# Kernel optimization log

Hardware: AMD Instinct MI355X
Metric: run time of the kernel (lower is better)

The kernel has to match this reference:

```python
import jax, jax.numpy as jnp
import numpy as np

N_NODES, N_EDGES = 16384, 8192
IN_CH, HID_CH = 256, 256
ALPHA, BETA = -1.5, -0.5


def setup_inputs() -> dict:
    key = jax.random.key(0)
    k1, k2, k3, k4, k5, k6 = jax.random.split(key, 6)
    x_0 = jax.random.normal(k1, (N_NODES, IN_CH), dtype=jnp.float32)
    # binary incidence matrix (n_nodes, n_edges)
    incidence_1 = jax.random.randint(k2, (N_NODES, N_EDGES), 0, 2).astype(jnp.float32)
    # conv weights (torch Conv: x @ W then neighborhood @ .)
    W0 = jax.random.normal(k3, (IN_CH, HID_CH), dtype=jnp.float32) * 0.02
    W1 = jax.random.normal(k4, (HID_CH, HID_CH), dtype=jnp.float32) * 0.02
    # xavier_uniform biases of shape (1, hidden)
    gain = 1.414
    bound = gain * np.sqrt(6.0 / (1 + HID_CH)) * np.sqrt(3.0) / np.sqrt(3.0)  # xavier bound = gain*sqrt(6/(fan_in+fan_out))
    bound = gain * np.sqrt(6.0 / (1 + HID_CH))
    bias_0_to_1 = jax.random.uniform(k5, (1, HID_CH), minval=-bound, maxval=bound, dtype=jnp.float32)
    bias_1_to_0 = jax.random.uniform(k6, (1, HID_CH), minval=-bound, maxval=bound, dtype=jnp.float32)
    return {"x_0": x_0, "incidence_1": incidence_1, "W0": W0, "W1": W1,
            "bias_0_to_1": bias_0_to_1, "bias_1_to_0": bias_1_to_0}


def _normalize_incidence(B1):
    # edge/node cardinalities raised to alpha/beta
    edge_card = jnp.sum(B1, axis=0) ** ALPHA          # (n_edges,)
    node_card = jnp.sum(B1, axis=1) ** BETA           # (n_nodes,)
    mask = (B1 > 0).astype(B1.dtype)
    d0_inv = 1.0 / (mask @ edge_card)                 # (n_nodes,) per-node sum of incident edge_card
    d1_inv = 1.0 / (mask.T @ node_card)               # (n_edges,) per-edge sum of member node_card
    # B1_norm = D0_left^-1 @ B1 @ diag(edge_card)
    B1_norm = d0_inv[:, None] * B1 * edge_card[None, :]
    # B1T_norm = D1_left^-1 @ B1^T @ diag(node_card)
    B1T_norm = d1_inv[:, None] * B1.T * node_card[None, :]
    return B1_norm, B1T_norm


def reference(x_0, incidence_1, W0, W1, bias_0_to_1, bias_1_to_0):
    B1_norm, B1T_norm = _normalize_incidence(incidence_1)
    # node -> edge conv: x_1 = B1T_norm @ (x_0 @ W0) + b01
    x_1 = B1T_norm @ (x_0 @ W0) + bias_0_to_1        # (n_edges, hid)
    # edge -> node conv: x_0 = B1_norm @ (x_1 @ W1) + b10
    x_0_out = B1_norm @ (x_1 @ W1) + bias_1_to_0     # (n_nodes, hid)
    return jax.nn.relu(x_0_out), jax.nn.relu(x_1)
```

## Files before the change

kernel.cpp:

```cpp
#include <hip/hip_runtime.h>
#include <stdint.h>

#define NN 16384
#define NE 8192
#define CH 256
#define MM1_SPLIT 8
#define MM2_SPLIT 4

typedef __attribute__((ext_vector_type(8))) short bf16x8;
typedef __attribute__((ext_vector_type(4))) float f32x4;

__device__ __forceinline__ unsigned short f2bf(float f) {
  unsigned u = __float_as_uint(f);
  u += 0x7FFFu + ((u >> 16) & 1u);
  return (unsigned short)(u >> 16);
}
__device__ __forceinline__ void async_copy16(const void* gptr, void* lptr) {
  __builtin_amdgcn_global_load_lds((const __attribute__((address_space(1))) unsigned int*)gptr,
                                   (__attribute__((address_space(3))) unsigned int*)lptr,
                                   16, 0, 0);
}

__device__ __forceinline__ void transpose32(unsigned* x) {
  const unsigned masks[5] = {0x0000FFFFu, 0x00FF00FFu, 0x0F0F0F0Fu, 0x33333333u, 0x55555555u};
#pragma unroll
  for (int jj = 0; jj < 5; ++jj) {
    const int j = 16 >> jj;
    const unsigned m = masks[jj];
#pragma unroll
    for (int k = 0; k < 32; ++k) {
      if ((k & j) == 0) {
        unsigned t = ((x[k] >> j) ^ x[k + j]) & m;
        x[k] ^= (t << j);
        x[k + j] ^= t;
      }
    }
  }
}

__global__ void k0_transpose_w(const float* __restrict__ W0, const float* __restrict__ W1,
                               unsigned short* __restrict__ W0T, unsigned short* __restrict__ W1T) {
  const float* W = blockIdx.y ? W1 : W0;
  unsigned short* WT = blockIdx.y ? W1T : W0T;
  int n = blockIdx.x;
  int k = threadIdx.x;
  WT[n * CH + k] = f2bf(W[k * CH + n]);
}

__global__ void k1_pack_card(const float* __restrict__ B1, unsigned* __restrict__ pk1,
                             float* __restrict__ node_card) {
  int n = blockIdx.x;
  int t = threadIdx.x;
  const float4* p = (const float4*)(B1 + (size_t)n * NE + t * 32);
  unsigned w = 0;
#pragma unroll
  for (int jj = 0; jj < 8; ++jj) {
    float4 v = p[jj];
    w |= ((__float_as_uint(v.x) >> 23) & 1u) << (4 * jj);
    w |= ((__float_as_uint(v.y) >> 23) & 1u) << (4 * jj + 1);
    w |= ((__float_as_uint(v.z) >> 23) & 1u) << (4 * jj + 2);
    w |= ((__float_as_uint(v.w) >> 23) & 1u) << (4 * jj + 3);
  }
  pk1[(size_t)n * 256 + t] = w;
  int s = __popc(w);
  __shared__ int red[4];
#pragma unroll
  for (int off = 32; off; off >>= 1) s += __shfl_down(s, off, 64);
  if ((t & 63) == 0) red[t >> 6] = s;
  __syncthreads();
  if (t == 0) {
    float tot = (float)(red[0] + red[1] + red[2] + red[3]);
    node_card[n] = rsqrtf(tot);
  }
}

__global__ __launch_bounds__(256) void k1b_bitT(const unsigned* __restrict__ pk1,
                                                unsigned* __restrict__ pk1T) {
  int bw = blockIdx.x & 127;
  int half = blockIdx.x >> 7;
  int t = threadIdx.x;
  int nt = half * 256 + t;
  unsigned x0[32], x1[32];
#pragma unroll
  for (int r = 0; r < 32; ++r) {
    uint2 v = *(const uint2*)&pk1[(size_t)(nt * 32 + r) * 256 + 2 * bw];
    x0[r] = v.x;
    x1[r] = v.y;
  }
  transpose32(x0);
  transpose32(x1);
  int e0 = bw * 64;
#pragma unroll
  for (int c = 0; c < 32; ++c) {
    pk1T[(size_t)(e0 + c) * 512 + nt] = x0[c];
    pk1T[(size_t)(e0 + 32 + c) * 512 + nt] = x1[c];
  }
}

__global__ void kcs_edge_card(const unsigned* __restrict__ pk1T, float* __restrict__ edge_card) {
  int lane = threadIdx.x & 63;
  int e = blockIdx.x * 4 + (threadIdx.x >> 6);
  const uint4* p = (const uint4*)(pk1T + (size_t)e * 512) + lane * 2;
  uint4 a = p[0], b = p[1];
  int s = __popc(a.x) + __popc(a.y) + __popc(a.z) + __popc(a.w) +
          __popc(b.x) + __popc(b.y) + __popc(b.z) + __popc(b.w);
#pragma unroll
  for (int off = 32; off; off >>= 1) s += __shfl_down(s, off, 64);
  if (lane == 0) {
    float cs = (float)s;
    edge_card[e] = 1.0f / (cs * sqrtf(cs));
  }
}

__global__ __launch_bounds__(256) void k2_y0(const float* __restrict__ X0,
                                             const unsigned short* __restrict__ W0T,
                                             const float* __restrict__ node_card,
                                             unsigned short* __restrict__ y0sT) {
  __shared__ __align__(16) unsigned short a_lds[64 * 32];
  __shared__ __align__(16) unsigned short b_lds[256 * 32];
  const int tid = threadIdx.x;
  const int wave = tid >> 6, lane = tid & 63;
  const int quad = lane >> 4, l15 = lane & 15;
  const int m0 = blockIdx.x * 64;
  const int ar = tid >> 3, ac = (tid & 7) * 4;

  f32x4 acc[4][4];
  const f32x4 fz = {0.f, 0.f, 0.f, 0.f};
#pragma unroll
  for (int i = 0; i < 4; ++i)
#pragma unroll
    for (int j = 0; j < 4; ++j) acc[i][j] = fz;

  for (int k0 = 0; k0 < CH; k0 += 32) {
    __syncthreads();
#pragma unroll
    for (int p = 0; p < 2; ++p) {
      float4 v = *(const float4*)(X0 + (size_t)(m0 + ar + p * 32) * CH + k0 + ac);
      uint2 w;
      w.x = ((unsigned)f2bf(v.x)) | ((unsigned)f2bf(v.y) << 16);
      w.y = ((unsigned)f2bf(v.z)) | ((unsigned)f2bf(v.w) << 16);
      *(uint2*)&a_lds[(ar + p * 32) * 32 + ac] = w;
    }
#pragma unroll
    for (int i = 0; i < 4; ++i) {
      int rowbase = wave * 64 + i * 16;
      const unsigned short* g = W0T + (size_t)(rowbase + (lane >> 2)) * CH + k0 + (lane & 3) * 8;
      async_copy16(g, &b_lds[rowbase * 32]);
    }
    __syncthreads();
    bf16x8 af[4];
#pragma unroll
    for (int i = 0; i < 4; ++i)
      af[i] = *(const bf16x8*)&a_lds[(i * 16 + l15) * 32 + quad * 8];
#pragma unroll
    for (int j = 0; j < 4; ++j) {
      bf16x8 bfr = *(const bf16x8*)&b_lds[(wave * 64 + j * 16 + l15) * 32 + quad * 8];
#pragma unroll
      for (int i = 0; i < 4; ++i)
        acc[i][j] = __builtin_amdgcn_mfma_f32_16x16x32_bf16(af[i], bfr, acc[i][j], 0, 0, 0);
    }
  }
#pragma unroll
  for (int i = 0; i < 4; ++i) {
    int row4 = m0 + i * 16 + quad * 4;
    float4 nc = *(const float4*)(node_card + row4);
#pragma unroll
    for (int j = 0; j < 4; ++j) {
      int col = wave * 64 + j * 16 + l15;
      f32x4 v = acc[i][j];
      ushort4 o;
      o.x = f2bf(v[0] * nc.x);
      o.y = f2bf(v[1] * nc.y);
      o.z = f2bf(v[2] * nc.z);
      o.w = f2bf(v[3] * nc.w);
      *(ushort4*)&y0sT[(size_t)col * NN + row4] = o;
    }
  }
}

__global__ void k2b_aux(const float* __restrict__ node_card, unsigned short* __restrict__ y0sT) {
  int n = blockIdx.x * 256 + threadIdx.x;
  y0sT[(size_t)256 * NN + n] = f2bf(node_card[n]);
#pragma unroll
  for (int r = 257; r < 272; ++r) y0sT[(size_t)r * NN + n] = 0;
}

__global__ __launch_bounds__(512, 4) void mm1_kernel(const unsigned char* __restrict__ pk1T,
                                                     const unsigned short* __restrict__ y0sT,
                                                     float* __restrict__ mm1p,
                                                     float* __restrict__ auxD) {
  __shared__ __align__(16) unsigned short a_lds[128 * 40];
  __shared__ __align__(16) unsigned short b_lds[272 * 32];
  const int tid = threadIdx.x;
  const int wave = tid >> 6, lane = tid & 63;
  const int quad = lane >> 4, l15 = lane & 15;
  const int wm = wave >> 2, wn = wave & 3;
  const int bid = blockIdx.x;
  const int sp = bid & 7;
  const int m0 = (bid >> 3) * 128;
  const int KS = NN / MM1_SPLIT;
  const int kbase = sp * KS;

  const int am = tid >> 2;
  const int akg = tid & 3;
  const int ajbs = akg ^ ((am >> 4) & 3);
  unsigned short* aw_dst = &a_lds[am * 40 + ajbs * 8];

  f32x4 acc[4][4];
  const f32x4 fz = {0.f, 0.f, 0.f, 0.f};
#pragma unroll
  for (int i = 0; i < 4; ++i)
#pragma unroll
    for (int j = 0; j < 4; ++j) acc[i][j] = fz;
  float daux = 0.f;

  const unsigned char* agp = pk1T + (size_t)(m0 + am) * (NN / 8) + (kbase >> 3) + akg;
  unsigned abyte = *agp;

  for (int kk = 0; kk < KS; kk += 32) {
    const int k0 = kbase + kk;
    const unsigned abcur = abyte;
    __syncthreads();
    {
      uint4 aw;
#pragma unroll
      for (int j = 0; j < 4; ++j) {
        unsigned lo = (abcur >> (2 * j)) & 1u;
        unsigned hi = (abcur >> (2 * j + 1)) & 1u;
        ((unsigned*)&aw)[j] = lo * 0x3F80u + hi * 0x3F800000u;
      }
      *(uint4*)aw_dst = aw;
    }
#pragma unroll
    for (int i = 0; i < 2; ++i) {
      int rowbase = wave * 32 + i * 16;
      const unsigned short* g = y0sT + (size_t)(rowbase + (lane >> 2)) * NN + k0 + (lane & 3) * 8;
      async_copy16(g, &b_lds[rowbase * 32]);
    }
    if (wave == 7) {
      const unsigned short* g = y0sT + (size_t)(256 + (lane >> 2)) * NN + k0 + (lane & 3) * 8;
      async_copy16(g, &b_lds[256 * 32]);
    }
    __syncthreads();
    if (kk + 32 < KS) {
      agp += 4;
      abyte = *agp;
    }
    {
      bf16x8 nc8 = *(const bf16x8*)&b_lds[256 * 32 + akg * 8];
      float part = 0.f;
#pragma unroll
      for (int j = 0; j < 8; ++j) {
        float ncf = __uint_as_float(((unsigned)(unsigned short)nc8[j]) << 16);
        part += ((abcur >> j) & 1u) ? ncf : 0.f;
      }
      daux += part;
    }
    bf16x8 af[4];
#pragma unroll
    for (int i = 0; i < 4; ++i) {
      int m = wm * 64 + i * 16 + l15;
      int jbs = quad ^ i;
      af[i] = *(const bf16x8*)&a_lds[m * 40 + jbs * 8];
    }
#pragma unroll
    for (int j = 0; j < 4; ++j) {
      bf16x8 bfr = *(const bf16x8*)&b_lds[(wn * 64 + j * 16 + l15) * 32 + quad * 8];
#pragma unroll
      for (int i = 0; i < 4; ++i)
        acc[i][j] = __builtin_amdgcn_mfma_f32_16x16x32_bf16(af[i], bfr, acc[i][j], 0, 0, 0);
    }
  }
  float* outp = mm1p + (size_t)sp * NE * CH;
#pragma unroll
  for (int i = 0; i < 4; ++i) {
    int row4 = m0 + wm * 64 + i * 16 + quad * 4;
#pragma unroll
    for (int j = 0; j < 4; ++j) {
      int col = wn * 64 + j * 16 + l15;
#pragma unroll
      for (int r = 0; r < 4; ++r) outp[(size_t)(row4 + r) * CH + col] = acc[i][j][r];
    }
  }
  __syncthreads();
  float* dred = (float*)a_lds;
  dred[tid] = daux;
  __syncthreads();
  if (tid < 128) {
    float s = dred[tid * 4] + dred[tid * 4 + 1] + dred[tid * 4 + 2] + dred[tid * 4 + 3];
    auxD[(size_t)sp * NE + m0 + tid] = s;
  }
}

__global__ void k3_edge_final(const float* __restrict__ mm1p, const float* __restrict__ auxD,
                              const float* __restrict__ b01,
                              float* __restrict__ out1, unsigned short* __restrict__ x1bf) {
  int e = blockIdx.x, c = threadIdx.x;
  float ds = 0.f, p = 0.f;
#pragma unroll
  for (int sp = 0; sp < MM1_SPLIT; ++sp) {
    ds += auxD[(size_t)sp * NE + e];
    p += mm1p[(size_t)sp * NE * CH + (size_t)e * CH + c];
  }
  float x1 = p / ds + b01[c];
  out1[(size_t)e * CH + c] = fmaxf(x1, 0.f);
  x1bf[(size_t)e * CH + c] = f2bf(x1);
}

__global__ __launch_bounds__(256) void k5_y1(const unsigned short* __restrict__ x1bf,
                                             const unsigned short* __restrict__ W1T,
                                             const float* __restrict__ edge_card,
                                             unsigned short* __restrict__ y1sT) {
  __shared__ __align__(16) unsigned short a_lds[64 * 32];
  __shared__ __align__(16) unsigned short b_lds[256 * 32];
  const int tid = threadIdx.x;
  const int wave = tid >> 6, lane = tid & 63;
  const int quad = lane >> 4, l15 = lane & 15;
  const int m0 = blockIdx.x * 64;

  f32x4 acc[4][4];
  const f32x4 fz = {0.f, 0.f, 0.f, 0.f};
#pragma unroll
  for (int i = 0; i < 4; ++i)
#pragma unroll
    for (int j = 0; j < 4; ++j) acc[i][j] = fz;

  for (int k0 = 0; k0 < CH; k0 += 32) {
    __syncthreads();
    {
      const unsigned short* g = x1bf + (size_t)(m0 + wave * 16 + (lane >> 2)) * CH + k0 + (lane & 3) * 8;
      async_copy16(g, &a_lds[(wave * 16) * 32]);
    }
#pragma unroll
    for (int i = 0; i < 4; ++i) {
      int rowbase = wave * 64 + i * 16;
      const unsigned short* g = W1T + (size_t)(rowbase + (lane >> 2)) * CH + k0 + (lane & 3) * 8;
      async_copy16(g, &b_lds[rowbase * 32]);
    }
    __syncthreads();
    bf16x8 af[4];
#pragma unroll
    for (int i = 0; i < 4; ++i)
      af[i] = *(const bf16x8*)&a_lds[(i * 16 + l15) * 32 + quad * 8];
#pragma unroll
    for (int j = 0; j < 4; ++j) {
      bf16x8 bfr = *(const bf16x8*)&b_lds[(wave * 64 + j * 16 + l15) * 32 + quad * 8];
#pragma unroll
      for (int i = 0; i < 4; ++i)
        acc[i][j] = __builtin_amdgcn_mfma_f32_16x16x32_bf16(af[i], bfr, acc[i][j], 0, 0, 0);
    }
  }
#pragma unroll
  for (int i = 0; i < 4; ++i) {
    int row4 = m0 + i * 16 + quad * 4;
    float4 ec = *(const float4*)(edge_card + row4);
#pragma unroll
    for (int j = 0; j < 4; ++j) {
      int col = wave * 64 + j * 16 + l15;
      f32x4 v = acc[i][j];
      ushort4 o;
      o.x = f2bf(v[0] * ec.x);
      o.y = f2bf(v[1] * ec.y);
      o.z = f2bf(v[2] * ec.z);
      o.w = f2bf(v[3] * ec.w);
      *(ushort4*)&y1sT[(size_t)col * NE + row4] = o;
    }
  }
}

__global__ void k5b_aux(const float* __restrict__ edge_card, unsigned short* __restrict__ y1sT) {
  int e = blockIdx.x * 256 + threadIdx.x;
  y1sT[(size_t)256 * NE + e] = f2bf(edge_card[e]);
#pragma unroll
  for (int r = 257; r < 272; ++r) y1sT[(size_t)r * NE + e] = 0;
}

__global__ __launch_bounds__(512, 4) void mm2_kernel(const unsigned char* __restrict__ pk1,
                                                     const unsigned short* __restrict__ y1sT,
                                                     float* __restrict__ mm2p,
                                                     float* __restrict__ d0p) {
  __shared__ __align__(16) unsigned short a_lds[128 * 40];
  __shared__ __align__(16) unsigned short b_lds[272 * 32];
  const int tid = threadIdx.x;
  const int wave = tid >> 6, lane = tid & 63;
  const int quad = lane >> 4, l15 = lane & 15;
  const int wm = wave >> 2, wn = wave & 3;
  const int bid = blockIdx.x;
  const int sp = (bid >> 1) & 3;
  const int m0 = (((bid >> 3) << 1) | (bid & 1)) * 128;
  const int KS = NE / MM2_SPLIT;
  const int kbase = sp * KS;

  const int am = tid >> 2;
  const int akg = tid & 3;
  const int ajbs = akg ^ ((am >> 4) & 3);
  unsigned short* aw_dst = &a_lds[am * 40 + ajbs * 8];

  f32x4 acc[4][4];
  const f32x4 fz = {0.f, 0.f, 0.f, 0.f};
#pragma unroll
  for (int i = 0; i < 4; ++i)
#pragma unroll
    for (int j = 0; j < 4; ++j) acc[i][j] = fz;
  float daux = 0.f;

  const unsigned char* agp = pk1 + (size_t)(m0 + am) * (NE / 8) + (kbase >> 3) + akg;
  unsigned abyte = *agp;

  for (int kk = 0; kk < KS; kk += 32) {
    const int k0 = kbase + kk;
    const unsigned abcur = abyte;
    __syncthreads();
    {
      uint4 aw;
#pragma unroll
      for (int j = 0; j < 4; ++j) {
        unsigned lo = (abcur >> (2 * j)) & 1u;
        unsigned hi = (abcur >> (2 * j + 1)) & 1u;
        ((unsigned*)&aw)[j] = lo * 0x3F80u + hi * 0x3F800000u;
      }
      *(uint4*)aw_dst = aw;
    }
#pragma unroll
    for (int i = 0; i < 2; ++i) {
      int rowbase = wave * 32 + i * 16;
      const unsigned short* g = y1sT + (size_t)(rowbase + (lane >> 2)) * NE + k0 + (lane & 3) * 8;
      async_copy16(g, &b_lds[rowbase * 32]);
    }
    if (wave == 7) {
      const unsigned short* g = y1sT + (size_t)(256 + (lane >> 2)) * NE + k0 + (lane & 3) * 8;
      async_copy16(g, &b_lds[256 * 32]);
    }
    __syncthreads();
    if (kk + 32 < KS) {
      agp += 4;
      abyte = *agp;
    }
    {
      bf16x8 ec8 = *(const bf16x8*)&b_lds[256 * 32 + akg * 8];
      float part = 0.f;
#pragma unroll
      for (int j = 0; j < 8; ++j) {
        float ecf = __uint_as_float(((unsigned)(unsigned short)ec8[j]) << 16);
        part += ((abcur >> j) & 1u) ? ecf : 0.f;
      }
      daux += part;
    }
    bf16x8 af[4];
#pragma unroll
    for (int i = 0; i < 4; ++i) {
      int m = wm * 64 + i * 16 + l15;
      int jbs = quad ^ i;
      af[i] = *(const bf16x8*)&a_lds[m * 40 + jbs * 8];
    }
#pragma unroll
    for (int j = 0; j < 4; ++j) {
      bf16x8 bfr = *(const bf16x8*)&b_lds[(wn * 64 + j * 16 + l15) * 32 + quad * 8];
#pragma unroll
      for (int i = 0; i < 4; ++i)
        acc[i][j] = __builtin_amdgcn_mfma_f32_16x16x32_bf16(af[i], bfr, acc[i][j], 0, 0, 0);
    }
  }
  float* outp = mm2p + (size_t)sp * NN * CH;
#pragma unroll
  for (int i = 0; i < 4; ++i) {
    int row4 = m0 + wm * 64 + i * 16 + quad * 4;
#pragma unroll
    for (int j = 0; j < 4; ++j) {
      int col = wn * 64 + j * 16 + l15;
#pragma unroll
      for (int r = 0; r < 4; ++r) outp[(size_t)(row4 + r) * CH + col] = acc[i][j][r];
    }
  }
  __syncthreads();
  float* dred = (float*)a_lds;
  dred[tid] = daux;
  __syncthreads();
  if (tid < 128) {
    float s = dred[tid * 4] + dred[tid * 4 + 1] + dred[tid * 4 + 2] + dred[tid * 4 + 3];
    d0p[(size_t)sp * NN + m0 + tid] = s;
  }
}

__global__ void k6_node_final(const float* __restrict__ mm2p, const float* __restrict__ d0p,
                              const float* __restrict__ b10, float* __restrict__ out0) {
  int n = blockIdx.x, c = threadIdx.x;
  float s = 0.f, d = 0.f;
#pragma unroll
  for (int sp = 0; sp < MM2_SPLIT; ++sp) {
    s += mm2p[(size_t)sp * NN * CH + (size_t)n * CH + c];
    d += d0p[(size_t)sp * NN + n];
  }
  float v = s / d + b10[c];
  out0[(size_t)n * CH + c] = fmaxf(v, 0.f);
}

extern "C" void kernel_launch(void* const* d_in, const int* in_sizes, int n_in,
                              void* d_out, int out_size, void* d_ws, size_t ws_size,
                              hipStream_t stream) {
  const float* x0 = (const float*)d_in[0];
  const float* B1 = (const float*)d_in[1];
  const float* W0 = (const float*)d_in[2];
  const float* W1 = (const float*)d_in[3];
  const float* b01 = (const float*)d_in[4];
  const float* b10 = (const float*)d_in[5];
  float* out0 = (float*)d_out;
  float* out1 = out0 + (size_t)NN * CH;

  char* ws = (char*)d_ws;
  size_t off = 0;
  auto take = [&](size_t bytes) {
    void* p = ws + off;
    off += (bytes + 255) & ~(size_t)255;
    return p;
  };
  unsigned short* y0sT = (unsigned short*)take((size_t)272 * NN * 2);
  unsigned short* y1sT = (unsigned short*)take((size_t)272 * NE * 2);
  unsigned short* x1bf = (unsigned short*)take((size_t)NE * CH * 2);
  float* mm1p = (float*)take((size_t)MM1_SPLIT * NE * CH * 4);
  float* mm2p = mm1p;
  float* node_card = (float*)take((size_t)NN * 4);
  float* edge_card = (float*)take((size_t)NE * 4);
  float* auxD = (float*)take((size_t)MM1_SPLIT * NE * 4);
  float* d0p = (float*)take((size_t)MM2_SPLIT * NN * 4);
  unsigned short* W0T = (unsigned short*)take((size_t)CH * CH * 2);
  unsigned short* W1T = (unsigned short*)take((size_t)CH * CH * 2);
  unsigned* pk1 = (unsigned*)take((size_t)NN * 256 * 4);
  unsigned* pk1T = (unsigned*)take((size_t)NE * 512 * 4);
  (void)ws_size; (void)in_sizes; (void)n_in; (void)out_size;

  k0_transpose_w<<<dim3(256, 2), 256, 0, stream>>>(W0, W1, W0T, W1T);
  k1_pack_card<<<NN, 256, 0, stream>>>(B1, pk1, node_card);
  k1b_bitT<<<256, 256, 0, stream>>>(pk1, pk1T);
  kcs_edge_card<<<NE / 4, 256, 0, stream>>>(pk1T, edge_card);
  k2_y0<<<NN / 64, 256, 0, stream>>>(x0, W0T, node_card, y0sT);
  k2b_aux<<<NN / 256, 256, 0, stream>>>(node_card, y0sT);
  mm1_kernel<<<512, 512, 0, stream>>>((const unsigned char*)pk1T, y0sT, mm1p, auxD);
  k3_edge_final<<<NE, 256, 0, stream>>>(mm1p, auxD, b01, out1, x1bf);
  k5_y1<<<NE / 64, 256, 0, stream>>>(x1bf, W1T, edge_card, y1sT);
  k5b_aux<<<NE / 256, 256, 0, stream>>>(edge_card, y1sT);
  mm2_kernel<<<512, 512, 0, stream>>>((const unsigned char*)pk1, y1sT, mm2p, d0p);
  k6_node_final<<<NN, 256, 0, stream>>>(mm2p, d0p, b10, out0);
}
```

Measured before the change: 977.2 us.

## Double-buffer LDS tiles in mm1/mm2 to overlap loads with MFMA

Converts both incidence-matmul kernels to a two-stage LDS pipeline. The next B tile is issued via async global-to-LDS copies and the next expanded A tile is written while MFMAs run on the current buffer, leaving one barrier per iteration instead of two. The padding-row zero stores in the aux kernels are also removed, since rows 257-271 are only consumed as unused MFMA columns. LDS use per block roughly doubles, which may lower occupancy. The async copy has no explicit wait before the barrier, so correctness depends on the barrier covering the in-flight loads.

```diff
diff --git a/kernel.cpp b/kernel.cpp
--- a/kernel.cpp
+++ b/kernel.cpp
@@ -19,6 +19,16 @@
   __builtin_amdgcn_global_load_lds((const __attribute__((address_space(1))) unsigned int*)gptr,
                                    (__attribute__((address_space(3))) unsigned int*)lptr,
                                    16, 0, 0);
+}
+__device__ __forceinline__ uint4 expand8(unsigned byte) {
+  uint4 aw;
+#pragma unroll
+  for (int j = 0; j < 4; ++j) {
+    unsigned lo = (byte >> (2 * j)) & 1u;
+    unsigned hi = (byte >> (2 * j + 1)) & 1u;
+    ((unsigned*)&aw)[j] = lo * 0x3F80u + hi * 0x3F800000u;
+  }
+  return aw;
 }
 
 __device__ __forceinline__ void transpose32(unsigned* x) {
@@ -181,16 +191,14 @@
 __global__ void k2b_aux(const float* __restrict__ node_card, unsigned short* __restrict__ y0sT) {
   int n = blockIdx.x * 256 + threadIdx.x;
   y0sT[(size_t)256 * NN + n] = f2bf(node_card[n]);
-#pragma unroll
-  for (int r = 257; r < 272; ++r) y0sT[(size_t)r * NN + n] = 0;
 }
 
 __global__ __launch_bounds__(512, 4) void mm1_kernel(const unsigned char* __restrict__ pk1T,
                                                      const unsigned short* __restrict__ y0sT,
                                                      float* __restrict__ mm1p,
                                                      float* __restrict__ auxD) {
-  __shared__ __align__(16) unsigned short a_lds[128 * 40];
-  __shared__ __align__(16) unsigned short b_lds[272 * 32];
+  __shared__ __align__(16) unsigned short a_lds[2][128 * 40];
+  __shared__ __align__(16) unsigned short b_lds[2][272 * 32];
   const int tid = threadIdx.x;
   const int wave = tid >> 6, lane = tid & 63;
   const int quad = lane >> 4, l15 = lane & 15;
@@ -199,12 +207,16 @@
   const int sp = bid & 7;
   const int m0 = (bid >> 3) * 128;
   const int KS = NN / MM1_SPLIT;
+  const int NT = KS / 32;
   const int kbase = sp * KS;
 
   const int am = tid >> 2;
   const int akg = tid & 3;
   const int ajbs = akg ^ ((am >> 4) & 3);
-  unsigned short* aw_dst = &a_lds[am * 40 + ajbs * 8];
+  const int aoff = am * 40 + ajbs * 8;
+
+  const int brow = lane >> 2;
+  const int bcol = (lane & 3) * 8;
 
   f32x4 acc[4][4];
   const f32x4 fz = {0.f, 0.f, 0.f, 0.f};
@@ -215,44 +227,51 @@
   float daux = 0.f;
 
   const unsigned char* agp = pk1T + (size_t)(m0 + am) * (NN / 8) + (kbase >> 3) + akg;
-  unsigned abyte = *agp;
-
-  for (int kk = 0; kk < KS; kk += 32) {
-    const int k0 = kbase + kk;
-    const unsigned abcur = abyte;
-    __syncthreads();
+  unsigned ab_cur = agp[0];
+  unsigned ab_nxt = agp[4];
+  const unsigned char* agq = agp + 8;
+
+#pragma unroll
+  for (int i = 0; i < 2; ++i) {
+    int rowbase = wave * 32 + i * 16;
+    const unsigned short* g = y0sT + (size_t)(rowbase + brow) * NN + kbase + bcol;
+    async_copy16(g, &b_lds[0][rowbase * 32]);
+  }
+  if (wave == 7) {
+    const unsigned short* g = y0sT + (size_t)(256 + brow) * NN + kbase + bcol;
+    async_copy16(g, &b_lds[0][256 * 32]);
+  }
+  *(uint4*)&a_lds[0][aoff] = expand8(ab_cur);
+  __syncthreads();
+
+  for (int t = 0; t < NT; ++t) {
+    const int cur = t & 1;
+    unsigned ab_new = 0;
+    if (t + 1 < NT) {
+      const int k0n = kbase + (t + 1) * 32;
+#pragma unroll
+      for (int i = 0; i < 2; ++i) {
+        int rowbase = wave * 32 + i * 16;
+        const unsigned short* g = y0sT + (size_t)(rowbase + brow) * NN + k0n + bcol;
+        async_copy16(g, &b_lds[cur ^ 1][rowbase * 32]);
+      }
+      if (wave == 7) {
+        const unsigned short* g = y0sT + (size_t)(256 + brow) * NN + k0n + bcol;
+        async_copy16(g, &b_lds[cur ^ 1][256 * 32]);
+      }
+      *(uint4*)&a_lds[cur ^ 1][aoff] = expand8(ab_nxt);
+      if (t + 2 < NT) {
+        ab_new = *agq;
+        agq += 4;
+      }
+    }
     {
-      uint4 aw;
-#pragma unroll
-      for (int j = 0; j < 4; ++j) {
-        unsigned lo = (abcur >> (2 * j)) & 1u;
-        unsigned hi = (abcur >> (2 * j + 1)) & 1u;
-        ((unsigned*)&aw)[j] = lo * 0x3F80u + hi * 0x3F800000u;
-      }
-      *(uint4*)aw_dst = aw;
-    }
-#pragma unroll
-    for (int i = 0; i < 2; ++i) {
-      int rowbase = wave * 32 + i * 16;
-      const unsigned short* g = y0sT + (size_t)(rowbase + (lane >> 2)) * NN + k0 + (lane & 3) * 8;
-      async_copy16(g, &b_lds[rowbase * 32]);
-    }
-    if (wave == 7) {
-      const unsigned short* g = y0sT + (size_t)(256 + (lane >> 2)) * NN + k0 + (lane & 3) * 8;
-      async_copy16(g, &b_lds[256 * 32]);
-    }
-    __syncthreads();
-    if (kk + 32 < KS) {
-      agp += 4;
-      abyte = *agp;
-    }
-    {
-      bf16x8 nc8 = *(const bf16x8*)&b_lds[256 * 32 + akg * 8];
+      bf16x8 nc8 = *(const bf16x8*)&b_lds[cur][256 * 32 + akg * 8];
       float part = 0.f;
 #pragma unroll
       for (int j = 0; j < 8; ++j) {
         float ncf = __uint_as_float(((unsigned)(unsigned short)nc8[j]) << 16);
-        part += ((abcur >> j) & 1u) ? ncf : 0.f;
+        part += ((ab_cur >> j) & 1u) ? ncf : 0.f;
       }
       daux += part;
     }
@@ -261,15 +280,18 @@
     for (int i = 0; i < 4; ++i) {
       int m = wm * 64 + i * 16 + l15;
       int jbs = quad ^ i;
-      af[i] = *(const bf16x8*)&a_lds[m * 40 + jbs * 8];
-    }
-#pragma unroll
-    for (int j = 0; j < 4; ++j) {
-      bf16x8 bfr = *(const bf16x8*)&b_lds[(wn * 64 + j * 16 + l15) * 32 + quad * 8];
+      af[i] = *(const bf16x8*)&a_lds[cur][m * 40 + jbs * 8];
+    }
+#pragma unroll
+    for (int j = 0; j < 4; ++j) {
+      bf16x8 bfr = *(const bf16x8*)&b_lds[cur][(wn * 64 + j * 16 + l15) * 32 + quad * 8];
 #pragma unroll
       for (int i = 0; i < 4; ++i)
         acc[i][j] = __builtin_amdgcn_mfma_f32_16x16x32_bf16(af[i], bfr, acc[i][j], 0, 0, 0);
     }
+    __syncthreads();
+    ab_cur = ab_nxt;
+    ab_nxt = ab_new;
   }
   float* outp = mm1p + (size_t)sp * NE * CH;
 #pragma unroll
@@ -371,16 +393,14 @@
 __global__ void k5b_aux(const float* __restrict__ edge_card, unsigned short* __restrict__ y1sT) {
   int e = blockIdx.x * 256 + threadIdx.x;
   y1sT[(size_t)256 * NE + e] = f2bf(edge_card[e]);
-#pragma unroll
-  for (int r = 257; r < 272; ++r) y1sT[(size_t)r * NE + e] = 0;
 }
 
 __global__ __launch_bounds__(512, 4) void mm2_kernel(const unsigned char* __restrict__ pk1,
                                                      const unsigned short* __restrict__ y1sT,
                                                      float* __restrict__ mm2p,
                                                      float* __restrict__ d0p) {
-  __shared__ __align__(16) unsigned short a_lds[128 * 40];
-  __shared__ __align__(16) unsigned short b_lds[272 * 32];
+  __shared__ __align__(16) unsigned short a_lds[2][128 * 40];
+  __shared__ __align__(16) unsigned short b_lds[2][272 * 32];
   const int tid = threadIdx.x;
   const int wave = tid >> 6, lane = tid & 63;
   const int quad = lane >> 4, l15 = lane & 15;
@@ -389,12 +409,15 @@
   const int sp = (bid >> 1) & 3;
   const int m0 = (((bid >> 3) << 1) | (bid & 1)) * 128;
   const int KS = NE / MM2_SPLIT;
+  const int NT = KS / 32;
   const int kbase = sp * KS;
 
   const int am = tid >> 2;
   const int akg = tid & 3;
   const int ajbs = akg ^ ((am >> 4) & 3);
-  unsigned short* aw_dst = &a_lds[am * 40 + ajbs * 8];
+  const int aoff = am * 40 + ajbs * 8;
+  const int brow = lane >> 2;
+  const int bcol = (lane & 3) * 8;
 
   f32x4 acc[4][4];
   const f32x4 fz = {0.f, 0.f, 0.f, 0.f};
@@ -405,44 +428,51 @@
   float daux = 0.f;
 
   const unsigned char* agp = pk1 + (size_t)(m0 + am) * (NE / 8) + (kbase >> 3) + akg;
-  unsigned abyte = *agp;
-
-  for (int kk = 0; kk < KS; kk += 32) {
-    const int k0 = kbase + kk;
-    const unsigned abcur = abyte;
-    __syncthreads();
+  unsigned ab_cur = agp[0];
+  unsigned ab_nxt = agp[4];
+  const unsigned char* agq = agp + 8;
+
+#pragma unroll
+  for (int i = 0; i < 2; ++i) {
+    int rowbase = wave * 32 + i * 16;
+    const unsigned short* g = y1sT + (size_t)(rowbase + brow) * NE + kbase + bcol;
+    async_copy16(g, &b_lds[0][rowbase * 32]);
+  }
+  if (wave == 7) {
+    const unsigned short* g = y1sT + (size_t)(256 + brow) * NE + kbase + bcol;
+    async_copy16(g, &b_lds[0][256 * 32]);
+  }
+  *(uint4*)&a_lds[0][aoff] = expand8(ab_cur);
+  __syncthreads();
+
+  for (int t = 0; t < NT; ++t) {
+    const int cur = t & 1;
+    unsigned ab_new = 0;
+    if (t + 1 < NT) {
+      const int k0n = kbase + (t + 1) * 32;
+#pragma unroll
+      for (int i = 0; i < 2; ++i) {
+        int rowbase = wave * 32 + i * 16;
+        const unsigned short* g = y1sT + (size_t)(rowbase + brow) * NE + k0n + bcol;
+        async_copy16(g, &b_lds[cur ^ 1][rowbase * 32]);
+      }
+      if (wave == 7) {
+        const unsigned short* g = y1sT + (size_t)(256 + brow) * NE + k0n + bcol;
+        async_copy16(g, &b_lds[cur ^ 1][256 * 32]);
+      }
+      *(uint4*)&a_lds[cur ^ 1][aoff] = expand8(ab_nxt);
+      if (t + 2 < NT) {
+        ab_new = *agq;
+        agq += 4;
+      }
+    }
     {
-      uint4 aw;
-#pragma unroll
-      for (int j = 0; j < 4; ++j) {
-        unsigned lo = (abcur >> (2 * j)) & 1u;
-        unsigned hi = (abcur >> (2 * j + 1)) & 1u;
-        ((unsigned*)&aw)[j] = lo * 0x3F80u + hi * 0x3F800000u;
-      }
-      *(uint4*)aw_dst = aw;
-    }
-#pragma unroll
-    for (int i = 0; i < 2; ++i) {
-      int rowbase = wave * 32 + i * 16;
-      const unsigned short* g = y1sT + (size_t)(rowbase + (lane >> 2)) * NE + k0 + (lane & 3) * 8;
-      async_copy16(g, &b_lds[rowbase * 32]);
-    }
-    if (wave == 7) {
-      const unsigned short* g = y1sT + (size_t)(256 + (lane >> 2)) * NE + k0 + (lane & 3) * 8;
-      async_copy16(g, &b_lds[256 * 32]);
-    }
-    __syncthreads();
-    if (kk + 32 < KS) {
-      agp += 4;
-      abyte = *agp;
-    }
-    {
-      bf16x8 ec8 = *(const bf16x8*)&b_lds[256 * 32 + akg * 8];
+      bf16x8 ec8 = *(const bf16x8*)&b_lds[cur][256 * 32 + akg * 8];
       float part = 0.f;
 #pragma unroll
       for (int j = 0; j < 8; ++j) {
         float ecf = __uint_as_float(((unsigned)(unsigned short)ec8[j]) << 16);
-        part += ((abcur >> j) & 1u) ? ecf : 0.f;
+        part += ((ab_cur >> j) & 1u) ? ecf : 0.f;
       }
       daux += part;
     }
@@ -451,15 +481,18 @@
     for (int i = 0; i < 4; ++i) {
       int m = wm * 64 + i * 16 + l15;
       int jbs = quad ^ i;
-      af[i] = *(const bf16x8*)&a_lds[m * 40 + jbs * 8];
-    }
-#pragma unroll
-    for (int j = 0; j < 4; ++j) {
-      bf16x8 bfr = *(const bf16x8*)&b_lds[(wn * 64 + j * 16 + l15) * 32 + quad * 8];
+      af[i] = *(const bf16x8*)&a_lds[cur][m * 40 + jbs * 8];
+    }
+#pragma unroll
+    for (int j = 0; j < 4; ++j) {
+      bf16x8 bfr = *(const bf16x8*)&b_lds[cur][(wn * 64 + j * 16 + l15) * 32 + quad * 8];
 #pragma unroll
       for (int i = 0; i < 4; ++i)
         acc[i][j] = __builtin_amdgcn_mfma_f32_16x16x32_bf16(af[i], bfr, acc[i][j], 0, 0, 0);
     }
+    __syncthreads();
+    ab_cur = ab_nxt;
+    ab_nxt = ab_new;
   }
   float* outp = mm2p + (size_t)sp * NN * CH;
 #pragma unroll
```

Result: no change. 974.0 us (-0.3%).
